# Kernel tuning notes

Measured on AMD Instinct MI355X. Metric: run time of the kernel, lower is better.

## Reference

```python
import jax, jax.numpy as jnp
import numpy as np

NUM_EXPERTS = 8
TOP_K = 2

def setup_inputs() -> dict:
    key = jax.random.key(0)
    k1, k2, k3, k4 = jax.random.split(key, 4)
    B, L, D, F, E = 2, 2048, 1024, 2048, NUM_EXPERTS
    layer_input = jax.random.normal(k1, (B, L, D), dtype=jnp.float32)
    router_w = jax.random.normal(k2, (E, D), dtype=jnp.float32) * 0.02
    # input_linear.weight.transpose(2,1) in torch -> [E, D, 2F] layout here
    w1 = jax.random.normal(k3, (E, D, 2 * F), dtype=jnp.float32) * 0.02
    # output_linear.weight.transpose(2,1) -> [E, F, D]
    w2 = jax.random.normal(k4, (E, F, D), dtype=jnp.float32) * 0.02
    return {"layer_input": layer_input, "router_w": router_w, "w1": w1, "w2": w2}


def reference(layer_input, router_w, w1, w2):
    B, L, D = layer_input.shape
    E = router_w.shape[0]
    x = layer_input.reshape(-1, D)                              # [N, D]
    router_logits = x @ router_w.T                              # [N, E]
    probs = jax.nn.softmax(router_logits.astype(jnp.float32), axis=-1)
    routing_weights, selected = jax.lax.top_k(probs, TOP_K)     # [N, K]
    routing_weights = routing_weights / routing_weights.sum(-1, keepdims=True)
    routing_weights = routing_weights.astype(x.dtype)

    out = jnp.zeros_like(x)
    # Fixed small loop over experts; same math as sorted grouped-GEMM + scatter-combine.
    for e in range(E):
        gate_e = jnp.sum(jnp.where(selected == e, routing_weights, 0.0), axis=-1)  # [N]
        gh = x @ w1[e]                                          # [N, 2F]
        g, h = jnp.split(gh, 2, axis=-1)
        y = (jax.nn.silu(g) * h) @ w2[e]                        # [N, D]
        out = out + gate_e[:, None] * y
    return out.reshape(B, L, D)
```

## Files before the change

### kernel.cpp

```cpp
#include <hip/hip_runtime.h>
#include <stdint.h>

typedef unsigned short u16;
typedef __attribute__((ext_vector_type(8))) short short8;
typedef __attribute__((ext_vector_type(4))) float floatx4;

#define NTOK 4096
#define DDIM 1024
#define FDIM 2048
#define NEXP 8

__device__ __forceinline__ u16 f2bf(float f) {
    union { float f; uint32_t u; } v; v.f = f;
    uint32_t r = v.u + 0x7fff + ((v.u >> 16) & 1);
    return (u16)(r >> 16);
}
__device__ __forceinline__ uint32_t pk2(float a, float b) {
    return (uint32_t)f2bf(a) | ((uint32_t)f2bf(b) << 16);
}
__device__ __forceinline__ void gl_lds16(const u16* g, u16* l) {
    __builtin_amdgcn_global_load_lds(
        (const __attribute__((address_space(1))) uint32_t*)g,
        (__attribute__((address_space(3))) uint32_t*)l, 16, 0, 0);
}

#define WAITV4 asm volatile("s_waitcnt vmcnt(4)" ::: "memory")
#define WAITV0 asm volatile("s_waitcnt vmcnt(0)" ::: "memory")
#define LGKM0  asm volatile("s_waitcnt lgkmcnt(0)" ::: "memory")
#define BAR    __builtin_amdgcn_s_barrier()
#define CFENCE asm volatile("" ::: "memory")

__global__ __launch_bounds__(256)
void router_kernel(const float* __restrict__ x, const float* __restrict__ rw,
                   int* __restrict__ topk_e, float* __restrict__ topk_w,
                   u16* __restrict__ xb) {
    const int lane = threadIdx.x & 63;
    const int wv = threadIdx.x >> 6;
    const int tok = blockIdx.x * 4 + wv;
    const float* xr = x + (size_t)tok * DDIM;
    u16* xo = xb + (size_t)tok * DDIM;
    float acc[8];
#pragma unroll
    for (int e = 0; e < 8; ++e) acc[e] = 0.f;
#pragma unroll
    for (int it = 0; it < 4; ++it) {
        int d0 = (it * 64 + lane) * 4;
        float4 xv = *(const float4*)(xr + d0);
        uint2 o = { pk2(xv.x, xv.y), pk2(xv.z, xv.w) };
        *(uint2*)(xo + d0) = o;
#pragma unroll
        for (int e = 0; e < 8; ++e) {
            float4 wv4 = *(const float4*)(rw + (size_t)e * DDIM + d0);
            acc[e] += xv.x * wv4.x + xv.y * wv4.y + xv.z * wv4.z + xv.w * wv4.w;
        }
    }
#pragma unroll
    for (int s = 32; s > 0; s >>= 1)
#pragma unroll
        for (int e = 0; e < 8; ++e) acc[e] += __shfl_down(acc[e], s);
    if (lane == 0) {
        int e0 = 0;
#pragma unroll
        for (int e = 1; e < 8; ++e) if (acc[e] > acc[e0]) e0 = e;
        int e1 = (e0 == 0) ? 1 : 0;
#pragma unroll
        for (int e = 0; e < 8; ++e) if (e != e0 && acc[e] > acc[e1]) e1 = e;
        float w0 = 1.f / (1.f + __expf(acc[e1] - acc[e0]));
        topk_e[tok * 2 + 0] = e0;
        topk_e[tok * 2 + 1] = e1;
        topk_w[tok * 2 + 0] = w0;
        topk_w[tok * 2 + 1] = 1.f - w0;
    }
}

__global__ __launch_bounds__(256)
void prefix_kernel(const int* __restrict__ topk_e, int* __restrict__ counts,
                   int* __restrict__ offs, int* __restrict__ cursors) {
    __shared__ int h[NEXP];
    const int t = threadIdx.x;
    if (t < NEXP) h[t] = 0;
    __syncthreads();
    int c[NEXP];
#pragma unroll
    for (int j = 0; j < NEXP; ++j) c[j] = 0;
    const int4* te4 = (const int4*)topk_e;
#pragma unroll
    for (int it = 0; it < 8; ++it) {
        int4 v = te4[it * 256 + t];
#pragma unroll
        for (int j = 0; j < NEXP; ++j)
            c[j] += (v.x == j) + (v.y == j) + (v.z == j) + (v.w == j);
    }
#pragma unroll
    for (int j = 0; j < NEXP; ++j)
        if (c[j]) atomicAdd(&h[j], c[j]);
    __syncthreads();
    if (t == 0) {
        int s = 0;
        for (int e = 0; e < NEXP; ++e) {
            counts[e] = h[e];
            offs[e] = s;
            s += h[e];
        }
        offs[NEXP] = s;
    }
    if (t < NEXP) cursors[t] = 0;
}

__global__ __launch_bounds__(256)
void build_rows(const int* __restrict__ topk_e, const int* __restrict__ offs,
                int* __restrict__ cursors, int* __restrict__ row_tok,
                float* __restrict__ gate_row, const float* __restrict__ topk_w) {
    __shared__ int lcnt[NEXP];
    __shared__ int lbase[NEXP];
    const int t = threadIdx.x;
    if (t < NEXP) lcnt[t] = 0;
    __syncthreads();
    const int tok = blockIdx.x * 256 + t;
    const int e0 = topk_e[tok * 2 + 0];
    const int e1 = topk_e[tok * 2 + 1];
    const int s0 = atomicAdd(&lcnt[e0], 1);
    const int s1 = atomicAdd(&lcnt[e1], 1);
    __syncthreads();
    if (t < NEXP) lbase[t] = lcnt[t] ? atomicAdd(&cursors[t], lcnt[t]) : 0;
    __syncthreads();
    int r0 = offs[e0] + lbase[e0] + s0;
    row_tok[r0] = tok;
    gate_row[r0] = topk_w[tok * 2 + 0];
    int r1 = offs[e1] + lbase[e1] + s1;
    row_tok[r1] = tok;
    gate_row[r1] = topk_w[tok * 2 + 1];
}

__global__ __launch_bounds__(256)
void transpose_f32_bf16(const float* __restrict__ src, u16* __restrict__ dst,
                        int R, int C) {
    __shared__ float tile[64][65];
    size_t eo = (size_t)blockIdx.z * R * C;
    const float* S = src + eo;
    u16* D = dst + eo;
    int r0 = blockIdx.y * 64, c0 = blockIdx.x * 64;
    int t = threadIdx.x;
    int rr = t >> 4;
    int cc = (t & 15) * 4;
#pragma unroll
    for (int it = 0; it < 4; ++it) {
        int r = rr + it * 16;
        float4 v = *(const float4*)(S + (size_t)(r0 + r) * C + (c0 + cc));
        tile[cc + 0][r] = v.x; tile[cc + 1][r] = v.y;
        tile[cc + 2][r] = v.z; tile[cc + 3][r] = v.w;
    }
    __syncthreads();
#pragma unroll
    for (int it = 0; it < 2; ++it) {
        int u = it * 256 + t;
        int c = u >> 3;
        int rv = (u & 7) * 8;
        uint4 o;
        o.x = pk2(tile[c][rv + 0], tile[c][rv + 1]);
        o.y = pk2(tile[c][rv + 2], tile[c][rv + 3]);
        o.z = pk2(tile[c][rv + 4], tile[c][rv + 5]);
        o.w = pk2(tile[c][rv + 6], tile[c][rv + 7]);
        *(uint4*)(D + (size_t)(c0 + c) * R + (r0 + rv)) = o;
    }
}

__global__ __launch_bounds__(256, 2)
void gemm1_fast(const u16* __restrict__ xb, const u16* __restrict__ w1b,
                u16* __restrict__ act, const int* __restrict__ row_tok,
                const int* __restrict__ counts, const int* __restrict__ offs) {
    const int bid = blockIdx.x;
    const int e = bid & 7;
    const int cnt = counts[e];
    const int nmb = (cnt + 127) >> 7;
    const int j = bid >> 3;
    if (j >= nmb * 32) return;
    const int m0 = (j % nmb) * 128;
    const int n0 = (j / nmb) * 64;
    const int off = offs[e];

    __shared__ __align__(16) u16 As[2 * 128 * 32];
    __shared__ __align__(16) u16 Bs[2 * 128 * 32];

    const int t = threadIdx.x;
    const int lane = t & 63;
    const int wv = t >> 6;
    const int quad = lane >> 4;
    const int rr = lane & 15;
    const int wm = (wv & 1) * 64;
    const int wn = (wv >> 1) * 32;

    const int scol = (lane & 3) * 8;
    const u16* arA[2];
    const u16* arB[2];
#pragma unroll
    for (int i = 0; i < 2; ++i) {
        int m = wv * 32 + i * 16 + ((lane >> 2) & 15);
        int r = m0 + m; if (r >= cnt) r = cnt - 1;
        arA[i] = xb + (size_t)row_tok[off + r] * DDIM + scol;
        size_t brow = (m < 64) ? ((size_t)e * 4096 + n0 + m)
                               : ((size_t)e * 4096 + 2048 + n0 + (m - 64));
        arB[i] = w1b + brow * DDIM + scol;
    }
    u16* dA0 = &As[(wv * 32) * 32];
    u16* dA1 = &As[(wv * 32 + 16) * 32];
    u16* dB0 = &Bs[(wv * 32) * 32];
    u16* dB1 = &Bs[(wv * 32 + 16) * 32];

    floatx4 accg[4][2] = {};
    floatx4 acch[4][2] = {};

#define G1_STAGE(b, ko)                                    \
    { gl_lds16(arA[0] + (ko), dA0 + (b) * 4096);           \
      gl_lds16(arA[1] + (ko), dA1 + (b) * 4096);           \
      gl_lds16(arB[0] + (ko), dB0 + (b) * 4096);           \
      gl_lds16(arB[1] + (ko), dB1 + (b) * 4096); }

#define G1_COMPUTE(b)                                                                   \
    { short8 af[4], bg[2], bh[2];                                                       \
      _Pragma("unroll") for (int mt = 0; mt < 4; ++mt)                                  \
          af[mt] = *(const short8*)&As[(b) * 4096 + (wm + mt * 16 + rr) * 32 + quad * 8];\
      _Pragma("unroll") for (int nt = 0; nt < 2; ++nt) {                                \
          bg[nt] = *(const short8*)&Bs[(b) * 4096 + (wn + nt * 16 + rr) * 32 + quad * 8];\
          bh[nt] = *(const short8*)&Bs[(b) * 4096 + (64 + wn + nt * 16 + rr) * 32 + quad * 8]; } \
      _Pragma("unroll") for (int mt = 0; mt < 4; ++mt)                                  \
          _Pragma("unroll") for (int nt = 0; nt < 2; ++nt) {                            \
              accg[mt][nt] = __builtin_amdgcn_mfma_f32_16x16x32_bf16(af[mt], bg[nt], accg[mt][nt], 0, 0, 0); \
              acch[mt][nt] = __builtin_amdgcn_mfma_f32_16x16x32_bf16(af[mt], bh[nt], acch[mt][nt], 0, 0, 0); } }

    G1_STAGE(0, 0);
    for (int p = 0; p < 15; ++p) {
        G1_STAGE(1, (2 * p + 1) * 32);
        WAITV4; BAR; CFENCE;
        G1_COMPUTE(0);
        LGKM0; BAR; CFENCE;
        G1_STAGE(0, (2 * p + 2) * 32);
        WAITV4; BAR; CFENCE;
        G1_COMPUTE(1);
        LGKM0; BAR; CFENCE;
    }
    G1_STAGE(1, 31 * 32);
    WAITV4; BAR; CFENCE;
    G1_COMPUTE(0);
    CFENCE;
    WAITV0; BAR; CFENCE;
    G1_COMPUTE(1);
#undef G1_STAGE
#undef G1_COMPUTE

#pragma unroll
    for (int mt = 0; mt < 4; ++mt)
#pragma unroll
        for (int nt = 0; nt < 2; ++nt)
#pragma unroll
            for (int rg = 0; rg < 4; ++rg) {
                int gm = m0 + wm + mt * 16 + quad * 4 + rg;
                if (gm < cnt) {
                    float g = accg[mt][nt][rg];
                    float h = acch[mt][nt][rg];
                    float s = g / (1.f + __expf(-g));
                    act[(size_t)(off + gm) * FDIM + (n0 + wn + nt * 16 + rr)] = f2bf(s * h);
                }
            }
}

__global__ __launch_bounds__(256, 2)
void gemm2_fast(const u16* __restrict__ act, const u16* __restrict__ w2b,
                float* __restrict__ out, const int* __restrict__ row_tok,
                const float* __restrict__ gate_row, const int* __restrict__ counts,
                const int* __restrict__ offs) {
    const int bid = blockIdx.x;
    const int e = bid & 7;
    const int cnt = counts[e];
    const int nmb = (cnt + 127) >> 7;
    const int j = bid >> 3;
    if (j >= nmb * 8) return;
    const int m0 = (j % nmb) * 128;
    const int n0 = (j / nmb) * 128;
    const int off = offs[e];

    __shared__ __align__(16) u16 As[2 * 128 * 32];
    __shared__ __align__(16) u16 Bs[2 * 128 * 32];

    const int t = threadIdx.x;
    const int lane = t & 63;
    const int wv = t >> 6;
    const int quad = lane >> 4;
    const int rr = lane & 15;
    const int wm = (wv & 1) * 64;
    const int wn = (wv >> 1) * 64;

    const int scol = (lane & 3) * 8;
    const u16* arA[2];
    const u16* arB[2];
#pragma unroll
    for (int i = 0; i < 2; ++i) {
        int m = wv * 32 + i * 16 + ((lane >> 2) & 15);
        int r = m0 + m; if (r >= cnt) r = cnt - 1;
        arA[i] = act + (size_t)(off + r) * FDIM + scol;
        arB[i] = w2b + ((size_t)e * 1024 + n0 + m) * FDIM + scol;
    }
    u16* dA0 = &As[(wv * 32) * 32];
    u16* dA1 = &As[(wv * 32 + 16) * 32];
    u16* dB0 = &Bs[(wv * 32) * 32];
    u16* dB1 = &Bs[(wv * 32 + 16) * 32];

    floatx4 acc[4][4] = {};

#define G2_STAGE(b, ko)                                    \
    { gl_lds16(arA[0] + (ko), dA0 + (b) * 4096);           \
      gl_lds16(arA[1] + (ko), dA1 + (b) * 4096);           \
      gl_lds16(arB[0] + (ko), dB0 + (b) * 4096);           \
      gl_lds16(arB[1] + (ko), dB1 + (b) * 4096); }

#define G2_COMPUTE(b)                                                                   \
    { short8 af[4], bf[4];                                                              \
      _Pragma("unroll") for (int mt = 0; mt < 4; ++mt)                                  \
          af[mt] = *(const short8*)&As[(b) * 4096 + (wm + mt * 16 + rr) * 32 + quad * 8];\
      _Pragma("unroll") for (int nt = 0; nt < 4; ++nt)                                  \
          bf[nt] = *(const short8*)&Bs[(b) * 4096 + (wn + nt * 16 + rr) * 32 + quad * 8];\
      _Pragma("unroll") for (int mt = 0; mt < 4; ++mt)                                  \
          _Pragma("unroll") for (int nt = 0; nt < 4; ++nt)                              \
              acc[mt][nt] = __builtin_amdgcn_mfma_f32_16x16x32_bf16(af[mt], bf[nt], acc[mt][nt], 0, 0, 0); }

    G2_STAGE(0, 0);
    for (int p = 0; p < 31; ++p) {
        G2_STAGE(1, (2 * p + 1) * 32);
        WAITV4; BAR; CFENCE;
        G2_COMPUTE(0);
        LGKM0; BAR; CFENCE;
        G2_STAGE(0, (2 * p + 2) * 32);
        WAITV4; BAR; CFENCE;
        G2_COMPUTE(1);
        LGKM0; BAR; CFENCE;
    }
    G2_STAGE(1, 63 * 32);
    WAITV4; BAR; CFENCE;
    G2_COMPUTE(0);
    CFENCE;
    WAITV0; BAR; CFENCE;
    G2_COMPUTE(1);
#undef G2_STAGE
#undef G2_COMPUTE

#pragma unroll
    for (int mt = 0; mt < 4; ++mt)
#pragma unroll
        for (int rg = 0; rg < 4; ++rg) {
            int gm = m0 + wm + mt * 16 + quad * 4 + rg;
            if (gm < cnt) {
                int gr = off + gm;
                float gate = gate_row[gr];
                float* orow = out + (size_t)row_tok[gr] * DDIM + n0 + wn;
#pragma unroll
                for (int nt = 0; nt < 4; ++nt)
                    atomicAdd(&orow[nt * 16 + rr], gate * acc[mt][nt][rg]);
            }
        }
}

extern "C" void kernel_launch(void* const* d_in, const int* in_sizes, int n_in,
                              void* d_out, int out_size, void* d_ws, size_t ws_size,
                              hipStream_t stream) {
    const float* x  = (const float*)d_in[0];
    const float* rw = (const float*)d_in[1];
    const float* w1 = (const float*)d_in[2];
    const float* w2 = (const float*)d_in[3];
    float* out = (float*)d_out;

    char* ws = (char*)d_ws;
    const size_t MB = 1ull << 20;
    int*   counts   = (int*)(ws);
    int*   cursors  = (int*)(ws + 64);
    int*   offs     = (int*)(ws + 128);
    int*   topk_e   = (int*)(ws + 2048);
    float* topk_w   = (float*)(ws + 2048 + 32768);
    int*   row_tok  = (int*)(ws + 2048 + 65536);
    float* gate_row = (float*)(ws + 2048 + 98304);
    u16*   act      = (u16*)(ws + 1 * MB);
    u16*   xb       = (u16*)(ws + 33 * MB);
    u16*   w1b      = (u16*)(ws + 41 * MB);
    u16*   w2b      = (u16*)(ws + 41 * MB);

    hipMemsetAsync(out, 0, (size_t)out_size * 4, stream);
    router_kernel<<<dim3(NTOK / 4), 256, 0, stream>>>(x, rw, topk_e, topk_w, xb);
    prefix_kernel<<<1, 256, 0, stream>>>(topk_e, counts, offs, cursors);
    build_rows<<<dim3(NTOK / 256), 256, 0, stream>>>(topk_e, offs, cursors, row_tok, gate_row, topk_w);
    transpose_f32_bf16<<<dim3(4096 / 64, 1024 / 64, NEXP), 256, 0, stream>>>(w1, w1b, 1024, 4096);
    gemm1_fast<<<dim3(8192), 256, 0, stream>>>(xb, w1b, act, row_tok, counts, offs);
    transpose_f32_bf16<<<dim3(1024 / 64, 2048 / 64, NEXP), 256, 0, stream>>>(w2, w2b, 2048, 1024);
    gemm2_fast<<<dim3(2048), 256, 0, stream>>>(act, w2b, out, row_tok, gate_row, counts, offs);
    (void)in_sizes; (void)n_in; (void)ws_size;
}
```

Before: 456.4 us.

## Swizzle LDS tiles in both expert GEMMs and halve barriers per k-step

```diff
diff --git a/kernel.cpp b/kernel.cpp
--- a/kernel.cpp
+++ b/kernel.cpp
@@ -24,11 +24,9 @@
         (__attribute__((address_space(3))) uint32_t*)l, 16, 0, 0);
 }
 
-#define WAITV4 asm volatile("s_waitcnt vmcnt(4)" ::: "memory")
 #define WAITV0 asm volatile("s_waitcnt vmcnt(0)" ::: "memory")
 #define LGKM0  asm volatile("s_waitcnt lgkmcnt(0)" ::: "memory")
 #define BAR    __builtin_amdgcn_s_barrier()
-#define CFENCE asm volatile("" ::: "memory")
 
 __global__ __launch_bounds__(256)
 void router_kernel(const float* __restrict__ x, const float* __restrict__ rw,
@@ -190,7 +188,8 @@
     const int wm = (wv & 1) * 64;
     const int wn = (wv >> 1) * 32;
 
-    const int scol = (lane & 3) * 8;
+    const int scol = (((lane & 3) ^ ((lane >> 3) & 3)) * 8);
+    const int xq = (quad ^ ((rr >> 1) & 3)) * 8;
     const u16* arA[2];
     const u16* arB[2];
 #pragma unroll
@@ -219,31 +218,28 @@
 #define G1_COMPUTE(b)                                                                   \
     { short8 af[4], bg[2], bh[2];                                                       \
       _Pragma("unroll") for (int mt = 0; mt < 4; ++mt)                                  \
-          af[mt] = *(const short8*)&As[(b) * 4096 + (wm + mt * 16 + rr) * 32 + quad * 8];\
+          af[mt] = *(const short8*)&As[(b) * 4096 + (wm + mt * 16 + rr) * 32 + xq];     \
       _Pragma("unroll") for (int nt = 0; nt < 2; ++nt) {                                \
-          bg[nt] = *(const short8*)&Bs[(b) * 4096 + (wn + nt * 16 + rr) * 32 + quad * 8];\
-          bh[nt] = *(const short8*)&Bs[(b) * 4096 + (64 + wn + nt * 16 + rr) * 32 + quad * 8]; } \
+          bg[nt] = *(const short8*)&Bs[(b) * 4096 + (wn + nt * 16 + rr) * 32 + xq];     \
+          bh[nt] = *(const short8*)&Bs[(b) * 4096 + (64 + wn + nt * 16 + rr) * 32 + xq]; } \
       _Pragma("unroll") for (int mt = 0; mt < 4; ++mt)                                  \
           _Pragma("unroll") for (int nt = 0; nt < 2; ++nt) {                            \
               accg[mt][nt] = __builtin_amdgcn_mfma_f32_16x16x32_bf16(af[mt], bg[nt], accg[mt][nt], 0, 0, 0); \
               acch[mt][nt] = __builtin_amdgcn_mfma_f32_16x16x32_bf16(af[mt], bh[nt], acch[mt][nt], 0, 0, 0); } }
 
     G1_STAGE(0, 0);
+    WAITV0; BAR;
     for (int p = 0; p < 15; ++p) {
         G1_STAGE(1, (2 * p + 1) * 32);
-        WAITV4; BAR; CFENCE;
         G1_COMPUTE(0);
-        LGKM0; BAR; CFENCE;
+        LGKM0; WAITV0; BAR;
         G1_STAGE(0, (2 * p + 2) * 32);
-        WAITV4; BAR; CFENCE;
         G1_COMPUTE(1);
-        LGKM0; BAR; CFENCE;
+        LGKM0; WAITV0; BAR;
     }
     G1_STAGE(1, 31 * 32);
-    WAITV4; BAR; CFENCE;
     G1_COMPUTE(0);
-    CFENCE;
-    WAITV0; BAR; CFENCE;
+    LGKM0; WAITV0; BAR;
     G1_COMPUTE(1);
 #undef G1_STAGE
 #undef G1_COMPUTE
@@ -290,7 +286,8 @@
     const int wm = (wv & 1) * 64;
     const int wn = (wv >> 1) * 64;
 
-    const int scol = (lane & 3) * 8;
+    const int scol = (((lane & 3) ^ ((lane >> 3) & 3)) * 8);
+    const int xq = (quad ^ ((rr >> 1) & 3)) * 8;
     const u16* arA[2];
     const u16* arB[2];
 #pragma unroll
@@ -316,29 +313,26 @@
 #define G2_COMPUTE(b)                                                                   \
     { short8 af[4], bf[4];                                                              \
       _Pragma("unroll") for (int mt = 0; mt < 4; ++mt)                                  \
-          af[mt] = *(const short8*)&As[(b) * 4096 + (wm + mt * 16 + rr) * 32 + quad * 8];\
+          af[mt] = *(const short8*)&As[(b) * 4096 + (wm + mt * 16 + rr) * 32 + xq];     \
       _Pragma("unroll") for (int nt = 0; nt < 4; ++nt)                                  \
-          bf[nt] = *(const short8*)&Bs[(b) * 4096 + (wn + nt * 16 + rr) * 32 + quad * 8];\
+          bf[nt] = *(const short8*)&Bs[(b) * 4096 + (wn + nt * 16 + rr) * 32 + xq];     \
       _Pragma("unroll") for (int mt = 0; mt < 4; ++mt)                                  \
           _Pragma("unroll") for (int nt = 0; nt < 4; ++nt)                              \
               acc[mt][nt] = __builtin_amdgcn_mfma_f32_16x16x32_bf16(af[mt], bf[nt], acc[mt][nt], 0, 0, 0); }
 
     G2_STAGE(0, 0);
+    WAITV0; BAR;
     for (int p = 0; p < 31; ++p) {
         G2_STAGE(1, (2 * p + 1) * 32);
-        WAITV4; BAR; CFENCE;
         G2_COMPUTE(0);
-        LGKM0; BAR; CFENCE;
+        LGKM0; WAITV0; BAR;
         G2_STAGE(0, (2 * p + 2) * 32);
-        WAITV4; BAR; CFENCE;
         G2_COMPUTE(1);
-        LGKM0; BAR; CFENCE;
+        LGKM0; WAITV0; BAR;
     }
     G2_STAGE(1, 63 * 32);
-    WAITV4; BAR; CFENCE;
     G2_COMPUTE(0);
-    CFENCE;
-    WAITV0; BAR; CFENCE;
+    LGKM0; WAITV0; BAR;
     G2_COMPUTE(1);
 #undef G2_STAGE
 #undef G2_COMPUTE
```

Result: no change. 450.8 us (-1.2%).
